# Optimization experiments

Hardware: AMD Instinct MI355X
Metric: run time of the kernel (lower is better)

Reference implementation:

```python
import jax, jax.numpy as jnp
import numpy as np

B, C, N, D, K, M, E, G = 2, 64, 16384, 3, 128, 1, 262144, 3


def setup_inputs() -> dict:
    key = jax.random.key(0)
    ks = jax.random.split(key, 15)
    scale = 1.0 / (C * C)
    return {
        "x": jax.random.normal(ks[0], (B, C, N), jnp.float32),
        "nodes": jax.random.uniform(ks[1], (B, N, D), jnp.float32),
        "node_weights": jax.random.uniform(ks[2], (B, N, M), jnp.float32),
        "geo": jax.random.normal(ks[3], (B, G, N), jnp.float32),
        "directed_edges": jax.random.randint(ks[4], (B, E, 2), 0, N, jnp.int32),
        "edge_gradient_weights": 0.1 * jax.random.normal(ks[5], (B, E, D), jnp.float32),
        "modes": jax.random.normal(ks[6], (K, D, M), jnp.float32),
        "weights_c": scale * jax.random.uniform(ks[7], (C, C, K, M), jnp.float32),
        "weights_s": scale * jax.random.uniform(ks[8], (C, C, K, M), jnp.float32),
        "weights_0": scale * jax.random.uniform(ks[9], (C, C, 1, M), jnp.float32),
        "W": jax.random.normal(ks[10], (C, C), jnp.float32) / np.sqrt(C),
        "gw": jax.random.normal(ks[11], (C, C * D), jnp.float32) / np.sqrt(C * D),
        "geo_wx": jax.random.normal(ks[12], (C, G), jnp.float32) / np.sqrt(G),
        "wx": jax.random.normal(ks[13], (C, C), jnp.float32) / np.sqrt(C),
        "w2": jax.random.normal(ks[14], (C, C), jnp.float32) / np.sqrt(C),
    }


def reference(x, nodes, node_weights, geo, directed_edges, edge_gradient_weights,
              modes, weights_c, weights_s, weights_0, W, gw, geo_wx, wx, w2):
    # ---- Fourier bases: cos(kx), sin(kx), 1 -------------------------------
    temp = jnp.einsum('bxd,kdw->bxkw', nodes, modes)          # [B,N,K,M]
    bases_c, bases_s = jnp.cos(temp), jnp.sin(temp)
    b, n = temp.shape[0], temp.shape[1]
    bases_0 = jnp.ones((b, n, 1, temp.shape[3]), temp.dtype)
    nw = node_weights[:, :, None, :]                          # quadrature weights
    wb_c, wb_s, wb_0 = bases_c * nw, bases_s * nw, bases_0 * nw

    # ---- Spectral convolution (non-uniform Fourier neural layer) ----------
    x_c = jnp.einsum('bix,bxkw->bikw', x, wb_c)
    x_s = -jnp.einsum('bix,bxkw->bikw', x, wb_s)
    x_0 = jnp.einsum('bix,bxkw->bikw', x, wb_0)
    f_c = jnp.einsum('bikw,iokw->bokw', x_c, weights_c) - jnp.einsum('bikw,iokw->bokw', x_s, weights_s)
    f_s = jnp.einsum('bikw,iokw->bokw', x_s, weights_c) + jnp.einsum('bikw,iokw->bokw', x_c, weights_s)
    f_0 = jnp.einsum('bikw,iokw->bokw', x_0, weights_0)
    x1 = (jnp.einsum('bokw,bxkw->box', f_0, bases_0)
          + 2.0 * jnp.einsum('bokw,bxkw->box', f_c, bases_c)
          - 2.0 * jnp.einsum('bokw,bxkw->box', f_s, bases_s))

    # ---- Pointwise linear W ----------------------------------------------
    x2 = jnp.einsum('oi,bix->box', W, x)

    # ---- Least-squares gradient via edge gather + scatter-add -------------
    fT = jnp.transpose(x, (0, 2, 1))                          # [B,N,C]
    tgt, src = directed_edges[..., 0], directed_edges[..., 1]  # [B,E]
    f_src = jnp.take_along_axis(fT, src[:, :, None], axis=1)   # [B,E,C]
    f_tgt = jnp.take_along_axis(fT, tgt[:, :, None], axis=1)
    df = f_src - f_tgt
    # message[b,e,c,d] = w[b,e,d] * df[b,e,c], flattened c-major -> [B,E,C*D]
    msg = (df[..., :, None] * edge_gradient_weights[..., None, :]).reshape(b, tgt.shape[1], -1)
    gradf = jnp.zeros((b, n, msg.shape[-1]), msg.dtype).at[jnp.arange(b)[:, None], tgt].add(msg)
    x3 = jnp.einsum('og,bng->bon', gw, gradf)                  # [B,C,N]

    # ---- Geo embedding: w2 @ (softsign(geo_wx@geo) * (wx@x)) --------------
    h = jax.nn.soft_sign(jnp.einsum('og,bgx->box', geo_wx, geo)) * jnp.einsum('oi,bix->box', wx, x)
    x4 = jnp.einsum('oi,bix->box', w2, h)

    return jax.nn.gelu(x1 + x2 + x3 + x4, approximate=False)
```

## Files before the change

kernel.cpp:

```cpp
#include <hip/hip_runtime.h>
#include <hip/hip_fp16.h>
#include <math.h>

#define BB 2
#define CC 64
#define NN 16384
#define DD 3
#define KK 128
#define EE 262144
#define GG 3
#define PP 128
#define PP2 64
#define LL (NN/PP)
#define KTOT 576

typedef short bf16x8 __attribute__((ext_vector_type(8)));
typedef float f32x4  __attribute__((ext_vector_type(4)));

__device__ __forceinline__ short f2bf(float f) {
    unsigned u = __float_as_uint(f);
    u += 0x7FFF + ((u >> 16) & 1);
    return (short)(u >> 16);
}
__device__ __forceinline__ float bf2f(unsigned short u) {
    return __uint_as_float(((unsigned)u) << 16);
}

constexpr size_t OFF_XB   = 0;
constexpr size_t OFF_PC   = OFF_XB   + (size_t)BB*NN*32;
constexpr size_t OFF_PS   = OFF_PC   + (size_t)BB*PP*CC*KK;
constexpr size_t OFF_BIN4 = OFF_PC;
constexpr size_t OFF_AC   = OFF_PS   + (size_t)BB*PP*CC*KK;
constexpr size_t OFF_AS   = OFF_AC   + (size_t)BB*CC*KK;
constexpr size_t OFF_F0   = OFF_AS   + (size_t)BB*CC*KK;
constexpr size_t OFF_X0   = OFF_F0   + (size_t)BB*CC;
constexpr size_t OFF_CNT  = OFF_X0   + (size_t)BB*CC;
constexpr size_t OFF_OFFS = OFF_CNT  + (size_t)BB*NN;
constexpr size_t OFF_RANK = OFF_OFFS + (size_t)BB*NN;
constexpr size_t OFF_GRB  = OFF_RANK + (size_t)BB*EE;
constexpr size_t OFF_APAN = OFF_GRB  + (size_t)BB*NN*96;
constexpr size_t OFF_GWXT = OFF_APAN + (size_t)BB*KTOT*CC/2;

#define S_B0 (BB*PP2*4)
#define S_B1 (S_B0 + (BB*EE)/256)
#define S_B2 (S_B1 + BB*(NN/64))
#define S_B3 (S_B2 + BB*CC)
#define S_B4 (S_B3 + 48)
__global__ void __launch_bounds__(256) k1(const float* __restrict__ x,
                                          const float* __restrict__ nwt,
                                          const int* __restrict__ edges,
                                          const float* __restrict__ W,
                                          const float* __restrict__ gw,
                                          const float* __restrict__ geo_wx,
                                          const float* __restrict__ w2,
                                          const float* __restrict__ nodes,
                                          const float* __restrict__ modes,
                                          unsigned short* __restrict__ xB,
                                          float* __restrict__ x0,
                                          int* __restrict__ counts,
                                          int* __restrict__ rank,
                                          float* __restrict__ gwxT,
                                          short* __restrict__ ApanB,
                                          float* __restrict__ pc,
                                          float* __restrict__ ps) {
    int blk = blockIdx.x;
    int tid = threadIdx.x;
    __shared__ __align__(16) char smem[36864];
    if (blk < S_B0) {
        short* Axw = (short*)smem;
        short* Bc  = (short*)(smem + 17408);
        short* Bsn = (short*)(smem + 17408 + 8704);
        float* ndl = (float*)(smem + 17408 + 8704 + 8704);
        int bc = blk;
        int b = bc >> 8;
        int rem = bc & 255;
        int chunk2 = rem >> 2;
        int kt = rem & 3;
        int k0 = kt * 32;
        int lane = tid & 63;
        int w = tid >> 6;
        int col = lane & 15;
        int quad = lane >> 4;
        int wk = w & 1;
        int wi = w >> 1;

        f32x4 ac[2], as4[2];
#pragma unroll
        for (int it = 0; it < 2; it++)
#pragma unroll
            for (int r = 0; r < 4; r++) { ac[it][r] = 0.f; as4[it][r] = 0.f; }

        for (int h = 0; h < 2; h++) {
            int nbase = chunk2*256 + h*128;
            if (h) __syncthreads();
            for (int e = tid; e < 128*3; e += 256) ndl[e] = nodes[((size_t)b*NN + nbase)*3 + e];
#pragma unroll
            for (int s = 0; s < 8; s++) {
                int e = tid + s*256;
                int i = e >> 5, seg = e & 31;
                float4 xv = *(const float4*)&x[((size_t)b*CC + i)*NN + nbase + seg*4];
                float4 wv = *(const float4*)&nwt[(size_t)b*NN + nbase + seg*4];
                unsigned lo = (unsigned)(unsigned short)f2bf(xv.x*wv.x)
                            | ((unsigned)(unsigned short)f2bf(xv.y*wv.y) << 16);
                unsigned hi = (unsigned)(unsigned short)f2bf(xv.z*wv.z)
                            | ((unsigned)(unsigned short)f2bf(xv.w*wv.w) << 16);
                *(uint2*)&Axw[i*136 + seg*4] = make_uint2(lo, hi);
            }
            __syncthreads();
#pragma unroll
            for (int s = 0; s < 16; s++) {
                int e = tid + s*256;
                int n = e & 127, kl = e >> 7;
                int k = k0 + kl;
                float t = ndl[n*3+0]*modes[k*3+0] + ndl[n*3+1]*modes[k*3+1]
                        + ndl[n*3+2]*modes[k*3+2];
                Bc [kl*136 + n] = f2bf(__cosf(t));
                Bsn[kl*136 + n] = f2bf(__sinf(t));
            }
            __syncthreads();

            int rowB = (wk*16 + col)*136;
#pragma unroll
            for (int ns = 0; ns < 4; ns++) {
                int koff = ns*32 + quad*8;
                bf16x8 bcf = *(bf16x8*)&Bc [rowB + koff];
                bf16x8 bsf = *(bf16x8*)&Bsn[rowB + koff];
#pragma unroll
                for (int it = 0; it < 2; it++) {
                    int itile = wi*2 + it;
                    bf16x8 af = *(bf16x8*)&Axw[(itile*16 + col)*136 + koff];
                    ac[it]  = __builtin_amdgcn_mfma_f32_16x16x32_bf16(af, bcf, ac[it], 0, 0, 0);
                    as4[it] = __builtin_amdgcn_mfma_f32_16x16x32_bf16(af, bsf, as4[it], 0, 0, 0);
                }
            }
        }
        int base = (b*PP2 + chunk2)*CC;
        int kw = k0 + wk*16 + col;
#pragma unroll
        for (int it = 0; it < 2; it++) {
#pragma unroll
            for (int r = 0; r < 4; r++) {
                int i = (wi*2 + it)*16 + quad*4 + r;
                pc[(size_t)(base + i)*KK + kw] = ac[it][r];
                ps[(size_t)(base + i)*KK + kw] = as4[it][r];
            }
        }
    } else if (blk < S_B1) {
        int idx = (blk - S_B0)*256 + tid;
        int tgt = edges[(size_t)idx*2 + 0];
        int b = idx / EE;
        rank[idx] = atomicAdd(&counts[b*NN + tgt], 1);
    } else if (blk < S_B2) {
        float (*tile)[65] = (float (*)[65])smem;
        int tb = blk - S_B1;
        int b = tb / (NN/64);
        int n0 = (tb % (NN/64)) * 64;
        int c = tid & 63, r4 = tid >> 6;
        for (int rr = 0; rr < 16; rr++) {
            int i = r4*16 + rr;
            tile[i][c] = x[((size_t)b*CC + i)*NN + n0 + c];
        }
        __syncthreads();
        for (int rr = 0; rr < 16; rr++) {
            int nn = r4*16 + rr;
            xB[((size_t)b*NN + n0 + nn)*64 + c] = (unsigned short)f2bf(tile[c][nn]);
        }
    } else if (blk < S_B3) {
        float* red = (float*)smem;
        int bi = blk - S_B2;
        int b = bi >> 6, i = bi & 63;
        const float4* __restrict__ xr = (const float4*)&x[((size_t)b*CC + i)*NN];
        const float4* __restrict__ wr = (const float4*)&nwt[(size_t)b*NN];
        float s = 0.f;
        for (int t = tid; t < NN/4; t += 256) {
            float4 xv = xr[t];
            float4 wv = wr[t];
            s += xv.x*wv.x + xv.y*wv.y + xv.z*wv.z + xv.w*wv.w;
        }
        red[tid] = s;
        __syncthreads();
        for (int off = 128; off > 0; off >>= 1) {
            if (tid < off) red[tid] += red[tid+off];
            __syncthreads();
        }
        if (tid == 0) x0[b*CC + i] = red[0];
    } else {
        int idx = (blk - S_B3)*256 + tid;
        if (idx < CC*CC) {
            int j = idx>>6, o = idx&63;
            short wv  = f2bf(W[o*CC+j]);
            short w2v = f2bf(w2[o*CC+j]);
            ApanB[((size_t)(0*CC+o))*KTOT + 256 + j] = wv;
            ApanB[((size_t)(1*CC+o))*KTOT + 256 + j] = wv;
            ApanB[((size_t)(0*CC+o))*KTOT + 320 + j] = w2v;
            ApanB[((size_t)(1*CC+o))*KTOT + 320 + j] = w2v;
        }
        if (idx < CC*CC*DD) {
            int g = idx>>6, o = idx&63;
            short gv = f2bf(gw[o*(CC*DD)+g]);
            ApanB[((size_t)(0*CC+o))*KTOT + 384 + g] = gv;
            ApanB[((size_t)(1*CC+o))*KTOT + 384 + g] = gv;
        }
        if (idx < GG*CC) { int g = idx>>6, i = idx&63; gwxT[idx] = geo_wx[i*GG+g]; }
    }
}

__global__ void __launch_bounds__(256) k2(const float* __restrict__ pc, const float* __restrict__ ps,
                                          float* __restrict__ Ac, float* __restrict__ As,
                                          const int* __restrict__ counts,
                                          int* __restrict__ offsets) {
    int blk = blockIdx.x;
    int tid = threadIdx.x;
    if (blk < 1024) {
        int idx = blk*16 + (tid >> 4);
        int sub = tid & 15;
        if (idx >= BB*CC*KK) return;
        int b = idx / (CC*KK);
        int r = idx % (CC*KK);
        float sc = 0.f, ss = 0.f;
        for (int ch = sub; ch < PP2; ch += 16) {
            size_t o = ((size_t)(b*PP2 + ch)*CC)*KK + r;
            sc += pc[o]; ss += ps[o];
        }
        sc += __shfl_xor(sc, 1); sc += __shfl_xor(sc, 2);
        sc += __shfl_xor(sc, 4); sc += __shfl_xor(sc, 8);
        ss += __shfl_xor(ss, 1); ss += __shfl_xor(ss, 2);
        ss += __shfl_xor(ss, 4); ss += __shfl_xor(ss, 8);
        if (sub == 0) { Ac[idx] = sc; As[idx] = ss; }
    } else {
        int b = blk - 1024;
        __shared__ int part[256];
        int base = b*NN + tid*64;
        int s = 0;
        for (int j = 0; j < 64; j++) s += counts[base + j];
        part[tid] = s;
        __syncthreads();
        for (int off = 1; off < 256; off <<= 1) {
            int v = (tid >= off) ? part[tid - off] : 0;
            __syncthreads();
            part[tid] += v;
            __syncthreads();
        }
        int excl = part[tid] - s;
        for (int j = 0; j < 64; j++) {
            int c = counts[base + j];
            offsets[base + j] = excl;
            excl += c;
        }
    }
}

__global__ void __launch_bounds__(256) k3(const float* __restrict__ Ac, const float* __restrict__ As_,
                                          const float* __restrict__ wc, const float* __restrict__ wsw,
                                          const float* __restrict__ w0, const float* __restrict__ x0,
                                          const int* __restrict__ edges, const float* __restrict__ egw,
                                          const int* __restrict__ offs, const int* __restrict__ rank,
                                          float4* __restrict__ bin4,
                                          short* __restrict__ ApanB, float* __restrict__ f0) {
    int idx = blockIdx.x;
    int tid = threadIdx.x;
    if (idx >= BB*CC*2) {
        int e = (idx - BB*CC*2)*256 + tid;
        int b = e / EE;
        int tgt = edges[(size_t)e*2+0];
        int src = edges[(size_t)e*2+1];
        const float* __restrict__ ew = &egw[(size_t)e*3];
        float e0 = ew[0], e1 = ew[1], e2 = ew[2];
        int pos = offs[b*NN+tgt] + rank[e];
        bin4[(size_t)b*EE + pos] = make_float4(__int_as_float(src), e0, e1, e2);
        return;
    }
    int b = idx / (CC*2);
    int rem = idx % (CC*2);
    int o = rem >> 1, khalf = rem & 1;
    int kl = tid & 63, ig = tid >> 6;
    int k = khalf*64 + kl;
    float fc = 0.f, fs = 0.f;
    for (int ii = 0; ii < 16; ii++) {
        int i = ig*16 + ii;
        float a_c = Ac[(b*CC+i)*KK + k];
        float a_s = As_[(b*CC+i)*KK + k];
        float wcc = wc[((size_t)(i*CC+o))*KK + k];
        float wss = wsw[((size_t)(i*CC+o))*KK + k];
        fc += a_c*wcc + a_s*wss;
        fs += a_c*wss - a_s*wcc;
    }
    __shared__ float rc[256], rs[256];
    __shared__ float f0s[64];
    rc[tid] = fc; rs[tid] = fs;
    if (khalf == 0 && tid < 64) f0s[tid] = x0[b*CC + tid] * w0[tid*CC + o];
    __syncthreads();
    if (ig == 0) {
        fc = rc[kl] + rc[64+kl] + rc[128+kl] + rc[192+kl];
        fs = rs[kl] + rs[64+kl] + rs[128+kl] + rs[192+kl];
        unsigned pk = (unsigned)(unsigned short)f2bf(2.f*fc)
                    | ((unsigned)(unsigned short)f2bf(-2.f*fs) << 16);
        ((unsigned*)ApanB)[((size_t)(b*CC + o))*(KTOT/2) + k] = pk;
    }
    if (khalf == 0 && tid == 0) {
        float acc = 0.f;
        for (int i = 0; i < 64; i++) acc += f0s[i];
        f0[b*CC+o] = acc;
    }
}

__global__ void __launch_bounds__(512, 8) k_eg(const unsigned short* __restrict__ xB,
                                               const int* __restrict__ offsets,
                                               const float4* __restrict__ bin4,
                                               const float* __restrict__ nodes,
                                               const float* __restrict__ modes,
                                               const float* __restrict__ geo,
                                               const short* __restrict__ ApanB,
                                               const float* __restrict__ f0,
                                               const float* __restrict__ wx,
                                               const float* __restrict__ gwxT,
                                               float* __restrict__ out) {
    int blk = blockIdx.x;
    int b  = blk >> 9;
    int n0 = (blk & 511) * 32;
    int tid = threadIdx.x;
    int lane = tid & 63;
    int w = tid >> 6;
    int wr = w >> 1;
    int wc = w & 1;
    int col  = lane & 15;
    int quad = lane >> 4;
    int quad8 = quad * 8;
    int quad4 = quad * 4;

    __shared__ __align__(16) char smem[37776];
    short* As = (short*)smem;
    short* Bs = (short*)(smem + 9216);
    short* Ws = (short*)(smem + 13824);
    unsigned short* gradfL = (unsigned short*)(smem + 23040);
    float* ndl  = (float*)(smem + 36864);
    float* geo3 = (float*)(smem + 37248);
    int* soff   = (int*)(smem + 37632);

    if (tid < 96) ndl[tid]  = nodes[((size_t)b*NN + n0)*3 + tid];
    if (tid < 96) geo3[tid] = geo[((size_t)b*GG + (tid >> 5))*NN + n0 + (tid & 31)];
    if (tid >= 128 && tid < 161) {
        int idx = n0 + tid - 128;
        soff[tid - 128] = (idx < NN) ? offsets[b*NN + idx] : EE;
    }
    for (int e = tid; e < 4096; e += 512) {
        int i = e >> 6, j = e & 63;
        Ws[i*72 + j] = f2bf(wx[i*64 + j]);
    }
    f32x4 acc, xwa;
#pragma unroll
    for (int r = 0; r < 4; r++) { acc[r] = f0[b*CC + wr*16 + quad4 + r]; xwa[r] = 0.f; }
    __syncthreads();

    const unsigned short* __restrict__ xBb = xB + (size_t)b*NN*64 + lane;
    const float4* __restrict__ binb = bin4 + (size_t)b*EE;
    for (int q = 0; q < 4; q++) {
        int nl = w*4 + q;
        int js = soff[nl], je = soff[nl+1];
        float a0 = 0.f, a1 = 0.f, a2 = 0.f, s0 = 0.f, s1 = 0.f, s2 = 0.f;
#pragma unroll 4
        for (int j = js; j < je; j++) {
            float4 e = binb[j];
            int src = __float_as_int(e.x);
            float xs = bf2f(xBb[(size_t)src*64]);
            a0 = fmaf(xs, e.y, a0);
            a1 = fmaf(xs, e.z, a1);
            a2 = fmaf(xs, e.w, a2);
            s0 += e.y; s1 += e.z; s2 += e.w;
        }
        float xtgt = bf2f(xBb[(size_t)(n0 + nl)*64]);
        float fv0 = a0 - xtgt*s0;
        float fv1 = a1 - xtgt*s1;
        float fv2 = a2 - xtgt*s2;
        int g0 = lane*3;
        gradfL[(g0>>6)*2304 + nl*72 + (g0&63)] = (unsigned short)f2bf(fv0);
        int g1 = g0 + 1;
        gradfL[(g1>>6)*2304 + nl*72 + (g1&63)] = (unsigned short)f2bf(fv1);
        int g2 = g0 + 2;
        gradfL[(g2>>6)*2304 + nl*72 + (g2&63)] = (unsigned short)f2bf(fv2);
    }

    const short* __restrict__ Ab = ApanB + ((size_t)b*CC)*KTOT;

    for (int c = 0; c < 9; c++) {
        __syncthreads();
        {
            int o = tid >> 3, seg = tid & 7;
            *(uint4*)&As[o*72 + seg*8] =
                *(const uint4*)&Ab[(size_t)o*KTOT + c*64 + seg*8];
        }
        if (c < 4) {
#pragma unroll
            for (int s = 0; s < 2; s++) {
                int e = tid + s*512;
                int n = e >> 5, kpl = e & 31;
                int kp = c*32 + kpl;
                float t = ndl[n*3+0]*modes[kp*3+0] + ndl[n*3+1]*modes[kp*3+1]
                        + ndl[n*3+2]*modes[kp*3+2];
                unsigned pk = (unsigned)(unsigned short)f2bf(__cosf(t))
                            | ((unsigned)(unsigned short)f2bf(__sinf(t)) << 16);
                ((unsigned*)Bs)[n*36 + kpl] = pk;
            }
        } else if (c == 4) {
            if (tid < 256) {
                int n = tid >> 3, seg = tid & 7;
                *(uint4*)&Bs[n*72 + seg*8] =
                    *(const uint4*)&xB[((size_t)(b*NN + n0 + n))*64 + seg*8];
            }
        } else if (c == 5) {
            int n = wc*16 + col;
            float gv0 = geo3[n], gv1 = geo3[32+n], gv2 = geo3[64+n];
#pragma unroll
            for (int r = 0; r < 4; r++) {
                int i = wr*16 + quad4 + r;
                float t = gwxT[i]*gv0 + gwxT[64+i]*gv1 + gwxT[128+i]*gv2;
                float ssv = t / (1.f + fabsf(t));
                Bs[n*72 + i] = f2bf(ssv * xwa[r]);
            }
        }
        __syncthreads();
        const short* Bbase = (c >= 6) ? (const short*)&gradfL[(size_t)(c-6)*2304] : Bs;
        int rowA = (wr*16 + col) * 72;
        int rowB = (wc*16 + col) * 72;
#pragma unroll
        for (int ko = 0; ko < 2; ko++) {
            int koff = ko*32 + quad8;
            bf16x8 af = *(bf16x8*)&As[rowA + koff];
            bf16x8 bfv = *(bf16x8*)&Bbase[rowB + koff];
            acc = __builtin_amdgcn_mfma_f32_16x16x32_bf16(af, bfv, acc, 0, 0, 0);
            if (c == 4) {
                bf16x8 wf = *(bf16x8*)&Ws[rowA + koff];
                xwa = __builtin_amdgcn_mfma_f32_16x16x32_bf16(wf, bfv, xwa, 0, 0, 0);
            }
        }
    }
#pragma unroll
    for (int r = 0; r < 4; r++) {
        int o = wr*16 + quad4 + r;
        float v = acc[r];
        float g = 0.5f * v * (1.f + erff(v * 0.70710678118654752f));
        out[((size_t)b*CC + o)*NN + n0 + wc*16 + col] = g;
    }
}

extern "C" void kernel_launch(void* const* d_in, const int* in_sizes, int n_in,
                              void* d_out, int out_size, void* d_ws, size_t ws_size,
                              hipStream_t stream) {
    const float* x      = (const float*)d_in[0];
    const float* nodes  = (const float*)d_in[1];
    const float* nwt    = (const float*)d_in[2];
    const float* geo    = (const float*)d_in[3];
    const int*   edges  = (const int*)d_in[4];
    const float* egw    = (const float*)d_in[5];
    const float* modes  = (const float*)d_in[6];
    const float* wc     = (const float*)d_in[7];
    const float* wsw    = (const float*)d_in[8];
    const float* w0     = (const float*)d_in[9];
    const float* W      = (const float*)d_in[10];
    const float* gw     = (const float*)d_in[11];
    const float* geo_wx = (const float*)d_in[12];
    const float* wx     = (const float*)d_in[13];
    const float* w2     = (const float*)d_in[14];

    float* ws   = (float*)d_ws;
    unsigned short* xB  = (unsigned short*)(ws + OFF_XB);
    float* pc   = ws + OFF_PC;
    float* ps   = ws + OFF_PS;
    float* Ac   = ws + OFF_AC;
    float* As_  = ws + OFF_AS;
    float* f0   = ws + OFF_F0;
    float* x0   = ws + OFF_X0;
    int*  counts = (int*)(ws + OFF_CNT);
    int*  offs   = (int*)(ws + OFF_OFFS);
    int*  rank   = (int*)(ws + OFF_RANK);
    float4* bin4 = (float4*)(ws + OFF_BIN4);
    short* ApanB  = (short*)(ws + OFF_APAN);
    float* gwxT   = ws + OFF_GWXT;
    float* out  = (float*)d_out;

    hipMemsetAsync(counts, 0, (size_t)(BB*NN)*sizeof(int), stream);

    k1 <<<S_B4, 256, 0, stream>>>(x, nwt, edges, W, gw, geo_wx, w2, nodes, modes,
                                  xB, x0, counts, rank, gwxT, ApanB, pc, ps);
    k2 <<<1024 + BB, 256, 0, stream>>>(pc, ps, Ac, As_, counts, offs);
    k3 <<<BB*CC*2 + (BB*EE)/256, 256, 0, stream>>>(Ac, As_, wc, wsw, w0, x0,
                                                   edges, egw, offs, rank, bin4, ApanB, f0);
    k_eg <<<BB*(NN/32), 512, 0, stream>>>(xB, offs, bin4, nodes, modes, geo,
                                          ApanB, f0, wx, gwxT, out);
}
```

Baseline: 181.7 us.

## Merge four kernel launches into one cooperative persistent kernel with grid syncs

```diff
diff --git a/kernel.cpp b/kernel.cpp
--- a/kernel.cpp
+++ b/kernel.cpp
@@ -1,6 +1,9 @@
 #include <hip/hip_runtime.h>
+#include <hip/hip_cooperative_groups.h>
 #include <hip/hip_fp16.h>
 #include <math.h>
+
+namespace cg = cooperative_groups;
 
 #define BB 2
 #define CC 64
@@ -9,9 +12,7 @@
 #define KK 128
 #define EE 262144
 #define GG 3
-#define PP 128
 #define PP2 64
-#define LL (NN/PP)
 #define KTOT 576
 
 typedef short bf16x8 __attribute__((ext_vector_type(8)));
@@ -28,9 +29,9 @@
 
 constexpr size_t OFF_XB   = 0;
 constexpr size_t OFF_PC   = OFF_XB   + (size_t)BB*NN*32;
-constexpr size_t OFF_PS   = OFF_PC   + (size_t)BB*PP*CC*KK;
+constexpr size_t OFF_PS   = OFF_PC   + (size_t)BB*128*CC*KK;
 constexpr size_t OFF_BIN4 = OFF_PC;
-constexpr size_t OFF_AC   = OFF_PS   + (size_t)BB*PP*CC*KK;
+constexpr size_t OFF_AC   = OFF_PS   + (size_t)BB*128*CC*KK;
 constexpr size_t OFF_AS   = OFF_AC   + (size_t)BB*CC*KK;
 constexpr size_t OFF_F0   = OFF_AS   + (size_t)BB*CC*KK;
 constexpr size_t OFF_X0   = OFF_F0   + (size_t)BB*CC;
@@ -41,405 +42,379 @@
 constexpr size_t OFF_APAN = OFF_GRB  + (size_t)BB*NN*96;
 constexpr size_t OFF_GWXT = OFF_APAN + (size_t)BB*KTOT*CC/2;
 
-#define S_B0 (BB*PP2*4)
-#define S_B1 (S_B0 + (BB*EE)/256)
-#define S_B2 (S_B1 + BB*(NN/64))
-#define S_B3 (S_B2 + BB*CC)
-#define S_B4 (S_B3 + 48)
-__global__ void __launch_bounds__(256) k1(const float* __restrict__ x,
-                                          const float* __restrict__ nwt,
-                                          const int* __restrict__ edges,
-                                          const float* __restrict__ W,
-                                          const float* __restrict__ gw,
-                                          const float* __restrict__ geo_wx,
-                                          const float* __restrict__ w2,
-                                          const float* __restrict__ nodes,
-                                          const float* __restrict__ modes,
-                                          unsigned short* __restrict__ xB,
-                                          float* __restrict__ x0,
-                                          int* __restrict__ counts,
-                                          int* __restrict__ rank,
-                                          float* __restrict__ gwxT,
-                                          short* __restrict__ ApanB,
-                                          float* __restrict__ pc,
-                                          float* __restrict__ ps) {
-    int blk = blockIdx.x;
-    int tid = threadIdx.x;
-    __shared__ __align__(16) char smem[36864];
-    if (blk < S_B0) {
-        short* Axw = (short*)smem;
-        short* Bc  = (short*)(smem + 17408);
-        short* Bsn = (short*)(smem + 17408 + 8704);
-        float* ndl = (float*)(smem + 17408 + 8704 + 8704);
-        int bc = blk;
-        int b = bc >> 8;
-        int rem = bc & 255;
-        int chunk2 = rem >> 2;
-        int kt = rem & 3;
-        int k0 = kt * 32;
-        int lane = tid & 63;
-        int w = tid >> 6;
-        int col = lane & 15;
-        int quad = lane >> 4;
-        int wk = w & 1;
-        int wi = w >> 1;
-
-        f32x4 ac[2], as4[2];
-#pragma unroll
-        for (int it = 0; it < 2; it++)
-#pragma unroll
-            for (int r = 0; r < 4; r++) { ac[it][r] = 0.f; as4[it][r] = 0.f; }
-
-        for (int h = 0; h < 2; h++) {
-            int nbase = chunk2*256 + h*128;
-            if (h) __syncthreads();
-            for (int e = tid; e < 128*3; e += 256) ndl[e] = nodes[((size_t)b*NN + nbase)*3 + e];
-#pragma unroll
-            for (int s = 0; s < 8; s++) {
-                int e = tid + s*256;
-                int i = e >> 5, seg = e & 31;
-                float4 xv = *(const float4*)&x[((size_t)b*CC + i)*NN + nbase + seg*4];
-                float4 wv = *(const float4*)&nwt[(size_t)b*NN + nbase + seg*4];
-                unsigned lo = (unsigned)(unsigned short)f2bf(xv.x*wv.x)
-                            | ((unsigned)(unsigned short)f2bf(xv.y*wv.y) << 16);
-                unsigned hi = (unsigned)(unsigned short)f2bf(xv.z*wv.z)
-                            | ((unsigned)(unsigned short)f2bf(xv.w*wv.w) << 16);
-                *(uint2*)&Axw[i*136 + seg*4] = make_uint2(lo, hi);
-            }
-            __syncthreads();
-#pragma unroll
-            for (int s = 0; s < 16; s++) {
-                int e = tid + s*256;
-                int n = e & 127, kl = e >> 7;
-                int k = k0 + kl;
-                float t = ndl[n*3+0]*modes[k*3+0] + ndl[n*3+1]*modes[k*3+1]
-                        + ndl[n*3+2]*modes[k*3+2];
-                Bc [kl*136 + n] = f2bf(__cosf(t));
-                Bsn[kl*136 + n] = f2bf(__sinf(t));
-            }
-            __syncthreads();
-
-            int rowB = (wk*16 + col)*136;
-#pragma unroll
-            for (int ns = 0; ns < 4; ns++) {
-                int koff = ns*32 + quad*8;
-                bf16x8 bcf = *(bf16x8*)&Bc [rowB + koff];
-                bf16x8 bsf = *(bf16x8*)&Bsn[rowB + koff];
-#pragma unroll
-                for (int it = 0; it < 2; it++) {
-                    int itile = wi*2 + it;
-                    bf16x8 af = *(bf16x8*)&Axw[(itile*16 + col)*136 + koff];
-                    ac[it]  = __builtin_amdgcn_mfma_f32_16x16x32_bf16(af, bcf, ac[it], 0, 0, 0);
-                    as4[it] = __builtin_amdgcn_mfma_f32_16x16x32_bf16(af, bsf, as4[it], 0, 0, 0);
-                }
-            }
-        }
-        int base = (b*PP2 + chunk2)*CC;
-        int kw = k0 + wk*16 + col;
-#pragma unroll
-        for (int it = 0; it < 2; it++) {
-#pragma unroll
-            for (int r = 0; r < 4; r++) {
-                int i = (wi*2 + it)*16 + quad*4 + r;
-                pc[(size_t)(base + i)*KK + kw] = ac[it][r];
-                ps[(size_t)(base + i)*KK + kw] = as4[it][r];
-            }
-        }
-    } else if (blk < S_B1) {
-        int idx = (blk - S_B0)*256 + tid;
-        int tgt = edges[(size_t)idx*2 + 0];
-        int b = idx / EE;
-        rank[idx] = atomicAdd(&counts[b*NN + tgt], 1);
-    } else if (blk < S_B2) {
-        float (*tile)[65] = (float (*)[65])smem;
-        int tb = blk - S_B1;
-        int b = tb / (NN/64);
-        int n0 = (tb % (NN/64)) * 64;
-        int c = tid & 63, r4 = tid >> 6;
-        for (int rr = 0; rr < 16; rr++) {
-            int i = r4*16 + rr;
-            tile[i][c] = x[((size_t)b*CC + i)*NN + n0 + c];
-        }
-        __syncthreads();
-        for (int rr = 0; rr < 16; rr++) {
-            int nn = r4*16 + rr;
-            xB[((size_t)b*NN + n0 + nn)*64 + c] = (unsigned short)f2bf(tile[c][nn]);
-        }
-    } else if (blk < S_B3) {
-        float* red = (float*)smem;
-        int bi = blk - S_B2;
-        int b = bi >> 6, i = bi & 63;
-        const float4* __restrict__ xr = (const float4*)&x[((size_t)b*CC + i)*NN];
-        const float4* __restrict__ wr = (const float4*)&nwt[(size_t)b*NN];
-        float s = 0.f;
-        for (int t = tid; t < NN/4; t += 256) {
-            float4 xv = xr[t];
-            float4 wv = wr[t];
-            s += xv.x*wv.x + xv.y*wv.y + xv.z*wv.z + xv.w*wv.w;
-        }
-        red[tid] = s;
-        __syncthreads();
-        for (int off = 128; off > 0; off >>= 1) {
-            if (tid < off) red[tid] += red[tid+off];
-            __syncthreads();
-        }
-        if (tid == 0) x0[b*CC + i] = red[0];
-    } else {
-        int idx = (blk - S_B3)*256 + tid;
-        if (idx < CC*CC) {
-            int j = idx>>6, o = idx&63;
-            short wv  = f2bf(W[o*CC+j]);
-            short w2v = f2bf(w2[o*CC+j]);
-            ApanB[((size_t)(0*CC+o))*KTOT + 256 + j] = wv;
-            ApanB[((size_t)(1*CC+o))*KTOT + 256 + j] = wv;
-            ApanB[((size_t)(0*CC+o))*KTOT + 320 + j] = w2v;
-            ApanB[((size_t)(1*CC+o))*KTOT + 320 + j] = w2v;
-        }
-        if (idx < CC*CC*DD) {
-            int g = idx>>6, o = idx&63;
-            short gv = f2bf(gw[o*(CC*DD)+g]);
-            ApanB[((size_t)(0*CC+o))*KTOT + 384 + g] = gv;
-            ApanB[((size_t)(1*CC+o))*KTOT + 384 + g] = gv;
-        }
-        if (idx < GG*CC) { int g = idx>>6, i = idx&63; gwxT[idx] = geo_wx[i*GG+g]; }
-    }
-}
-
-__global__ void __launch_bounds__(256) k2(const float* __restrict__ pc, const float* __restrict__ ps,
-                                          float* __restrict__ Ac, float* __restrict__ As,
-                                          const int* __restrict__ counts,
-                                          int* __restrict__ offsets) {
-    int blk = blockIdx.x;
-    int tid = threadIdx.x;
-    if (blk < 1024) {
-        int idx = blk*16 + (tid >> 4);
-        int sub = tid & 15;
-        if (idx >= BB*CC*KK) return;
-        int b = idx / (CC*KK);
-        int r = idx % (CC*KK);
-        float sc = 0.f, ss = 0.f;
-        for (int ch = sub; ch < PP2; ch += 16) {
-            size_t o = ((size_t)(b*PP2 + ch)*CC)*KK + r;
-            sc += pc[o]; ss += ps[o];
-        }
-        sc += __shfl_xor(sc, 1); sc += __shfl_xor(sc, 2);
-        sc += __shfl_xor(sc, 4); sc += __shfl_xor(sc, 8);
-        ss += __shfl_xor(ss, 1); ss += __shfl_xor(ss, 2);
-        ss += __shfl_xor(ss, 4); ss += __shfl_xor(ss, 8);
-        if (sub == 0) { Ac[idx] = sc; As[idx] = ss; }
-    } else {
-        int b = blk - 1024;
-        __shared__ int part[256];
-        int base = b*NN + tid*64;
-        int s = 0;
-        for (int j = 0; j < 64; j++) s += counts[base + j];
-        part[tid] = s;
-        __syncthreads();
-        for (int off = 1; off < 256; off <<= 1) {
-            int v = (tid >= off) ? part[tid - off] : 0;
-            __syncthreads();
-            part[tid] += v;
-            __syncthreads();
-        }
-        int excl = part[tid] - s;
-        for (int j = 0; j < 64; j++) {
-            int c = counts[base + j];
-            offsets[base + j] = excl;
-            excl += c;
-        }
-    }
-}
-
-__global__ void __launch_bounds__(256) k3(const float* __restrict__ Ac, const float* __restrict__ As_,
-                                          const float* __restrict__ wc, const float* __restrict__ wsw,
-                                          const float* __restrict__ w0, const float* __restrict__ x0,
-                                          const int* __restrict__ edges, const float* __restrict__ egw,
-                                          const int* __restrict__ offs, const int* __restrict__ rank,
-                                          float4* __restrict__ bin4,
-                                          short* __restrict__ ApanB, float* __restrict__ f0) {
-    int idx = blockIdx.x;
-    int tid = threadIdx.x;
-    if (idx >= BB*CC*2) {
-        int e = (idx - BB*CC*2)*256 + tid;
-        int b = e / EE;
-        int tgt = edges[(size_t)e*2+0];
-        int src = edges[(size_t)e*2+1];
-        const float* __restrict__ ew = &egw[(size_t)e*3];
-        float e0 = ew[0], e1 = ew[1], e2 = ew[2];
-        int pos = offs[b*NN+tgt] + rank[e];
-        bin4[(size_t)b*EE + pos] = make_float4(__int_as_float(src), e0, e1, e2);
-        return;
-    }
-    int b = idx / (CC*2);
-    int rem = idx % (CC*2);
-    int o = rem >> 1, khalf = rem & 1;
-    int kl = tid & 63, ig = tid >> 6;
-    int k = khalf*64 + kl;
-    float fc = 0.f, fs = 0.f;
-    for (int ii = 0; ii < 16; ii++) {
-        int i = ig*16 + ii;
-        float a_c = Ac[(b*CC+i)*KK + k];
-        float a_s = As_[(b*CC+i)*KK + k];
-        float wcc = wc[((size_t)(i*CC+o))*KK + k];
-        float wss = wsw[((size_t)(i*CC+o))*KK + k];
-        fc += a_c*wcc + a_s*wss;
-        fs += a_c*wss - a_s*wcc;
-    }
-    __shared__ float rc[256], rs[256];
-    __shared__ float f0s[64];
-    rc[tid] = fc; rs[tid] = fs;
-    if (khalf == 0 && tid < 64) f0s[tid] = x0[b*CC + tid] * w0[tid*CC + o];
-    __syncthreads();
-    if (ig == 0) {
-        fc = rc[kl] + rc[64+kl] + rc[128+kl] + rc[192+kl];
-        fs = rs[kl] + rs[64+kl] + rs[128+kl] + rs[192+kl];
-        unsigned pk = (unsigned)(unsigned short)f2bf(2.f*fc)
-                    | ((unsigned)(unsigned short)f2bf(-2.f*fs) << 16);
-        ((unsigned*)ApanB)[((size_t)(b*CC + o))*(KTOT/2) + k] = pk;
-    }
-    if (khalf == 0 && tid == 0) {
-        float acc = 0.f;
-        for (int i = 0; i < 64; i++) acc += f0s[i];
-        f0[b*CC+o] = acc;
-    }
-}
-
-__global__ void __launch_bounds__(512, 8) k_eg(const unsigned short* __restrict__ xB,
-                                               const int* __restrict__ offsets,
-                                               const float4* __restrict__ bin4,
-                                               const float* __restrict__ nodes,
-                                               const float* __restrict__ modes,
-                                               const float* __restrict__ geo,
-                                               const short* __restrict__ ApanB,
-                                               const float* __restrict__ f0,
-                                               const float* __restrict__ wx,
-                                               const float* __restrict__ gwxT,
-                                               float* __restrict__ out) {
-    int blk = blockIdx.x;
-    int b  = blk >> 9;
-    int n0 = (blk & 511) * 32;
+#define U_KA  (BB*PP2*4)
+#define U_ED  ((BB*EE)/512)
+#define U_TR  (BB*(NN/64))
+#define U_X0  (BB*CC)
+#define U_WT  24
+#define U1 (U_KA + U_ED + U_TR + U_X0 + U_WT)
+#define U2 (512 + BB)
+#define U3 (BB*CC + (BB*EE)/512)
+#define U4 (BB*(NN/32))
+
+__global__ void __launch_bounds__(512, 8)
+mega(const float* __restrict__ x, const float* __restrict__ nwt,
+     const int* __restrict__ edges, const float* __restrict__ egw,
+     const float* __restrict__ W, const float* __restrict__ gw,
+     const float* __restrict__ geo_wx, const float* __restrict__ w2,
+     const float* __restrict__ nodes, const float* __restrict__ modes,
+     const float* __restrict__ geo, const float* __restrict__ wcw,
+     const float* __restrict__ wsw, const float* __restrict__ w0,
+     const float* __restrict__ wx,
+     unsigned short* __restrict__ xB, float* __restrict__ x0v,
+     int* __restrict__ counts, int* __restrict__ rank,
+     float* __restrict__ gwxT, short* __restrict__ ApanB,
+     float* __restrict__ pc, float* __restrict__ ps,
+     float* __restrict__ Ac, float* __restrict__ As_,
+     float* __restrict__ f0, int* __restrict__ offsets,
+     float4* __restrict__ bin4, float* __restrict__ out) {
+    cg::grid_group gridg = cg::this_grid();
+    int NB = gridDim.x;
     int tid = threadIdx.x;
     int lane = tid & 63;
     int w = tid >> 6;
-    int wr = w >> 1;
-    int wc = w & 1;
-    int col  = lane & 15;
-    int quad = lane >> 4;
-    int quad8 = quad * 8;
-    int quad4 = quad * 4;
-
     __shared__ __align__(16) char smem[37776];
-    short* As = (short*)smem;
-    short* Bs = (short*)(smem + 9216);
-    short* Ws = (short*)(smem + 13824);
-    unsigned short* gradfL = (unsigned short*)(smem + 23040);
-    float* ndl  = (float*)(smem + 36864);
-    float* geo3 = (float*)(smem + 37248);
-    int* soff   = (int*)(smem + 37632);
-
-    if (tid < 96) ndl[tid]  = nodes[((size_t)b*NN + n0)*3 + tid];
-    if (tid < 96) geo3[tid] = geo[((size_t)b*GG + (tid >> 5))*NN + n0 + (tid & 31)];
-    if (tid >= 128 && tid < 161) {
-        int idx = n0 + tid - 128;
-        soff[tid - 128] = (idx < NN) ? offsets[b*NN + idx] : EE;
-    }
-    for (int e = tid; e < 4096; e += 512) {
-        int i = e >> 6, j = e & 63;
-        Ws[i*72 + j] = f2bf(wx[i*64 + j]);
-    }
-    f32x4 acc, xwa;
-#pragma unroll
-    for (int r = 0; r < 4; r++) { acc[r] = f0[b*CC + wr*16 + quad4 + r]; xwa[r] = 0.f; }
-    __syncthreads();
-
-    const unsigned short* __restrict__ xBb = xB + (size_t)b*NN*64 + lane;
-    const float4* __restrict__ binb = bin4 + (size_t)b*EE;
-    for (int q = 0; q < 4; q++) {
-        int nl = w*4 + q;
-        int js = soff[nl], je = soff[nl+1];
-        float a0 = 0.f, a1 = 0.f, a2 = 0.f, s0 = 0.f, s1 = 0.f, s2 = 0.f;
-#pragma unroll 4
-        for (int j = js; j < je; j++) {
-            float4 e = binb[j];
-            int src = __float_as_int(e.x);
-            float xs = bf2f(xBb[(size_t)src*64]);
-            a0 = fmaf(xs, e.y, a0);
-            a1 = fmaf(xs, e.z, a1);
-            a2 = fmaf(xs, e.w, a2);
-            s0 += e.y; s1 += e.z; s2 += e.w;
-        }
-        float xtgt = bf2f(xBb[(size_t)(n0 + nl)*64]);
-        float fv0 = a0 - xtgt*s0;
-        float fv1 = a1 - xtgt*s1;
-        float fv2 = a2 - xtgt*s2;
-        int g0 = lane*3;
-        gradfL[(g0>>6)*2304 + nl*72 + (g0&63)] = (unsigned short)f2bf(fv0);
-        int g1 = g0 + 1;
-        gradfL[(g1>>6)*2304 + nl*72 + (g1&63)] = (unsigned short)f2bf(fv1);
-        int g2 = g0 + 2;
-        gradfL[(g2>>6)*2304 + nl*72 + (g2&63)] = (unsigned short)f2bf(fv2);
-    }
-
-    const short* __restrict__ Ab = ApanB + ((size_t)b*CC)*KTOT;
-
-    for (int c = 0; c < 9; c++) {
+
+    for (int u = blockIdx.x; u < U1; u += NB) {
         __syncthreads();
-        {
-            int o = tid >> 3, seg = tid & 7;
-            *(uint4*)&As[o*72 + seg*8] =
-                *(const uint4*)&Ab[(size_t)o*KTOT + c*64 + seg*8];
-        }
-        if (c < 4) {
-#pragma unroll
-            for (int s = 0; s < 2; s++) {
-                int e = tid + s*512;
-                int n = e >> 5, kpl = e & 31;
-                int kp = c*32 + kpl;
-                float t = ndl[n*3+0]*modes[kp*3+0] + ndl[n*3+1]*modes[kp*3+1]
-                        + ndl[n*3+2]*modes[kp*3+2];
-                unsigned pk = (unsigned)(unsigned short)f2bf(__cosf(t))
-                            | ((unsigned)(unsigned short)f2bf(__sinf(t)) << 16);
-                ((unsigned*)Bs)[n*36 + kpl] = pk;
-            }
-        } else if (c == 4) {
-            if (tid < 256) {
-                int n = tid >> 3, seg = tid & 7;
-                *(uint4*)&Bs[n*72 + seg*8] =
-                    *(const uint4*)&xB[((size_t)(b*NN + n0 + n))*64 + seg*8];
-            }
-        } else if (c == 5) {
-            int n = wc*16 + col;
-            float gv0 = geo3[n], gv1 = geo3[32+n], gv2 = geo3[64+n];
+        if (u < U_KA) {
+            short* Axw = (short*)smem;
+            short* Bc  = (short*)(smem + 17408);
+            short* Bsn = (short*)(smem + 17408 + 8704);
+            float* ndl = (float*)(smem + 17408 + 8704 + 8704);
+            int b = u >> 8;
+            int rem = u & 255;
+            int chunk2 = rem >> 2;
+            int kt = rem & 3;
+            int k0 = kt * 32;
+            int col = lane & 15;
+            int quad = lane >> 4;
+            int wk = w & 1;
+            int wi = w >> 1;
+            f32x4 ac, as4;
+#pragma unroll
+            for (int r = 0; r < 4; r++) { ac[r] = 0.f; as4[r] = 0.f; }
+            for (int h = 0; h < 2; h++) {
+                int nbase = chunk2*256 + h*128;
+                if (h) __syncthreads();
+                for (int e = tid; e < 384; e += 512) ndl[e] = nodes[((size_t)b*NN + nbase)*3 + e];
+#pragma unroll
+                for (int s = 0; s < 4; s++) {
+                    int e = tid + s*512;
+                    int i = e >> 5, seg = e & 31;
+                    float4 xv = *(const float4*)&x[((size_t)b*CC + i)*NN + nbase + seg*4];
+                    float4 wv = *(const float4*)&nwt[(size_t)b*NN + nbase + seg*4];
+                    unsigned lo = (unsigned)(unsigned short)f2bf(xv.x*wv.x)
+                                | ((unsigned)(unsigned short)f2bf(xv.y*wv.y) << 16);
+                    unsigned hi = (unsigned)(unsigned short)f2bf(xv.z*wv.z)
+                                | ((unsigned)(unsigned short)f2bf(xv.w*wv.w) << 16);
+                    *(uint2*)&Axw[i*136 + seg*4] = make_uint2(lo, hi);
+                }
+                __syncthreads();
+#pragma unroll
+                for (int s = 0; s < 8; s++) {
+                    int e = tid + s*512;
+                    int n = e & 127, kl = e >> 7;
+                    int k = k0 + kl;
+                    float t = ndl[n*3+0]*modes[k*3+0] + ndl[n*3+1]*modes[k*3+1]
+                            + ndl[n*3+2]*modes[k*3+2];
+                    Bc [kl*136 + n] = f2bf(__cosf(t));
+                    Bsn[kl*136 + n] = f2bf(__sinf(t));
+                }
+                __syncthreads();
+                int rowB = (wk*16 + col)*136;
+#pragma unroll
+                for (int ns = 0; ns < 4; ns++) {
+                    int koff = ns*32 + quad*8;
+                    bf16x8 bcf = *(bf16x8*)&Bc [rowB + koff];
+                    bf16x8 bsf = *(bf16x8*)&Bsn[rowB + koff];
+                    bf16x8 af = *(bf16x8*)&Axw[(wi*16 + col)*136 + koff];
+                    ac  = __builtin_amdgcn_mfma_f32_16x16x32_bf16(af, bcf, ac, 0, 0, 0);
+                    as4 = __builtin_amdgcn_mfma_f32_16x16x32_bf16(af, bsf, as4, 0, 0, 0);
+                }
+            }
+            int base = (b*PP2 + chunk2)*CC;
+            int kw = k0 + wk*16 + col;
 #pragma unroll
             for (int r = 0; r < 4; r++) {
-                int i = wr*16 + quad4 + r;
-                float t = gwxT[i]*gv0 + gwxT[64+i]*gv1 + gwxT[128+i]*gv2;
-                float ssv = t / (1.f + fabsf(t));
-                Bs[n*72 + i] = f2bf(ssv * xwa[r]);
-            }
-        }
-        __syncthreads();
-        const short* Bbase = (c >= 6) ? (const short*)&gradfL[(size_t)(c-6)*2304] : Bs;
-        int rowA = (wr*16 + col) * 72;
-        int rowB = (wc*16 + col) * 72;
-#pragma unroll
-        for (int ko = 0; ko < 2; ko++) {
-            int koff = ko*32 + quad8;
-            bf16x8 af = *(bf16x8*)&As[rowA + koff];
-            bf16x8 bfv = *(bf16x8*)&Bbase[rowB + koff];
-            acc = __builtin_amdgcn_mfma_f32_16x16x32_bf16(af, bfv, acc, 0, 0, 0);
-            if (c == 4) {
-                bf16x8 wf = *(bf16x8*)&Ws[rowA + koff];
-                xwa = __builtin_amdgcn_mfma_f32_16x16x32_bf16(wf, bfv, xwa, 0, 0, 0);
-            }
+                int i = wi*16 + quad*4 + r;
+                pc[(size_t)(base + i)*KK + kw] = ac[r];
+                ps[(size_t)(base + i)*KK + kw] = as4[r];
+            }
+        } else if (u < U_KA + U_ED) {
+            int idx = (u - U_KA)*512 + tid;
+            int tgt = edges[(size_t)idx*2 + 0];
+            int b = idx / EE;
+            rank[idx] = atomicAdd(&counts[b*NN + tgt], 1);
+        } else if (u < U_KA + U_ED + U_TR) {
+            float (*tile)[65] = (float (*)[65])smem;
+            int tb = u - (U_KA + U_ED);
+            int b = tb / (NN/64);
+            int n0 = (tb % (NN/64)) * 64;
+            int c = tid & 63, r8 = tid >> 6;
+            for (int rr = 0; rr < 8; rr++) {
+                int i = r8*8 + rr;
+                tile[i][c] = x[((size_t)b*CC + i)*NN + n0 + c];
+            }
+            __syncthreads();
+            for (int rr = 0; rr < 8; rr++) {
+                int nn = r8*8 + rr;
+                xB[((size_t)b*NN + n0 + nn)*64 + c] = (unsigned short)f2bf(tile[c][nn]);
+            }
+        } else if (u < U_KA + U_ED + U_TR + U_X0) {
+            float* red = (float*)smem;
+            int bi = u - (U_KA + U_ED + U_TR);
+            int b = bi >> 6, i = bi & 63;
+            const float4* __restrict__ xr = (const float4*)&x[((size_t)b*CC + i)*NN];
+            const float4* __restrict__ wr = (const float4*)&nwt[(size_t)b*NN];
+            float s = 0.f;
+            for (int t = tid; t < NN/4; t += 512) {
+                float4 xv = xr[t];
+                float4 wv = wr[t];
+                s += xv.x*wv.x + xv.y*wv.y + xv.z*wv.z + xv.w*wv.w;
+            }
+            red[tid] = s;
+            __syncthreads();
+            for (int off = 256; off > 0; off >>= 1) {
+                if (tid < off) red[tid] += red[tid+off];
+                __syncthreads();
+            }
+            if (tid == 0) x0v[b*CC + i] = red[0];
+        } else {
+            int idx = (u - (U_KA + U_ED + U_TR + U_X0))*512 + tid;
+            if (idx < CC*CC) {
+                int j = idx>>6, o = idx&63;
+                short wv  = f2bf(W[o*CC+j]);
+                short w2v = f2bf(w2[o*CC+j]);
+                ApanB[((size_t)(0*CC+o))*KTOT + 256 + j] = wv;
+                ApanB[((size_t)(1*CC+o))*KTOT + 256 + j] = wv;
+                ApanB[((size_t)(0*CC+o))*KTOT + 320 + j] = w2v;
+                ApanB[((size_t)(1*CC+o))*KTOT + 320 + j] = w2v;
+            }
+            if (idx < CC*CC*DD) {
+                int g = idx>>6, o = idx&63;
+                short gv = f2bf(gw[o*(CC*DD)+g]);
+                ApanB[((size_t)(0*CC+o))*KTOT + 384 + g] = gv;
+                ApanB[((size_t)(1*CC+o))*KTOT + 384 + g] = gv;
+            }
+            if (idx < GG*CC) { int g = idx>>6, i = idx&63; gwxT[idx] = geo_wx[i*GG+g]; }
         }
     }
-#pragma unroll
-    for (int r = 0; r < 4; r++) {
-        int o = wr*16 + quad4 + r;
-        float v = acc[r];
-        float g = 0.5f * v * (1.f + erff(v * 0.70710678118654752f));
-        out[((size_t)b*CC + o)*NN + n0 + wc*16 + col] = g;
+    gridg.sync();
+
+    for (int u = blockIdx.x; u < U2; u += NB) {
+        __syncthreads();
+        if (u < 512) {
+            int idx = u*32 + (tid >> 4);
+            int sub = tid & 15;
+            int b = idx / (CC*KK);
+            int r = idx % (CC*KK);
+            float sc = 0.f, ss = 0.f;
+            for (int ch = sub; ch < PP2; ch += 16) {
+                size_t o = ((size_t)(b*PP2 + ch)*CC)*KK + r;
+                sc += pc[o]; ss += ps[o];
+            }
+            sc += __shfl_xor(sc, 1); sc += __shfl_xor(sc, 2);
+            sc += __shfl_xor(sc, 4); sc += __shfl_xor(sc, 8);
+            ss += __shfl_xor(ss, 1); ss += __shfl_xor(ss, 2);
+            ss += __shfl_xor(ss, 4); ss += __shfl_xor(ss, 8);
+            if (sub == 0) { Ac[idx] = sc; As_[idx] = ss; }
+        } else {
+            int b = u - 512;
+            int* part = (int*)smem;
+            int base = b*NN + tid*32;
+            int s = 0;
+            for (int j = 0; j < 32; j++) s += counts[base + j];
+            part[tid] = s;
+            __syncthreads();
+            for (int off = 1; off < 512; off <<= 1) {
+                int v = (tid >= off) ? part[tid - off] : 0;
+                __syncthreads();
+                part[tid] += v;
+                __syncthreads();
+            }
+            int excl = part[tid] - s;
+            for (int j = 0; j < 32; j++) {
+                int c = counts[base + j];
+                offsets[base + j] = excl;
+                excl += c;
+            }
+        }
+    }
+    gridg.sync();
+
+    for (int u = blockIdx.x; u < U3; u += NB) {
+        __syncthreads();
+        if (u < BB*CC) {
+            float* rc  = (float*)smem;
+            float* rs  = (float*)(smem + 2048);
+            float* f0s = (float*)(smem + 4096);
+            int b = u >> 6, o = u & 63;
+            int khalf = tid >> 8;
+            int t2 = tid & 255;
+            int kl = t2 & 63, ig = t2 >> 6;
+            int k = khalf*64 + kl;
+            float fc = 0.f, fs = 0.f;
+            for (int ii = 0; ii < 16; ii++) {
+                int i = ig*16 + ii;
+                float a_c = Ac[(b*CC+i)*KK + k];
+                float a_s = As_[(b*CC+i)*KK + k];
+                float wcc = wcw[((size_t)(i*CC+o))*KK + k];
+                float wss = wsw[((size_t)(i*CC+o))*KK + k];
+                fc += a_c*wcc + a_s*wss;
+                fs += a_c*wss - a_s*wcc;
+            }
+            rc[tid] = fc; rs[tid] = fs;
+            if (tid < 64) f0s[tid] = x0v[b*CC + tid] * w0[tid*CC + o];
+            __syncthreads();
+            if (ig == 0) {
+                int tb = khalf*256;
+                fc = rc[tb+kl] + rc[tb+64+kl] + rc[tb+128+kl] + rc[tb+192+kl];
+                fs = rs[tb+kl] + rs[tb+64+kl] + rs[tb+128+kl] + rs[tb+192+kl];
+                unsigned pk = (unsigned)(unsigned short)f2bf(2.f*fc)
+                            | ((unsigned)(unsigned short)f2bf(-2.f*fs) << 16);
+                ((unsigned*)ApanB)[((size_t)(b*CC + o))*(KTOT/2) + k] = pk;
+            }
+            if (tid == 0) {
+                float acc2 = 0.f;
+                for (int i = 0; i < 64; i++) acc2 += f0s[i];
+                f0[b*CC+o] = acc2;
+            }
+        } else {
+            int e = (u - BB*CC)*512 + tid;
+            int b = e / EE;
+            int tgt = edges[(size_t)e*2+0];
+            int src = edges[(size_t)e*2+1];
+            const float* __restrict__ ew = &egw[(size_t)e*3];
+            float e0 = ew[0], e1 = ew[1], e2 = ew[2];
+            int pos = offsets[b*NN+tgt] + rank[e];
+            bin4[(size_t)b*EE + pos] = make_float4(__int_as_float(src), e0, e1, e2);
+        }
+    }
+    gridg.sync();
+
+    {
+        short* As = (short*)smem;
+        short* Bs = (short*)(smem + 9216);
+        short* Ws = (short*)(smem + 13824);
+        unsigned short* gradfL = (unsigned short*)(smem + 23040);
+        float* ndl  = (float*)(smem + 36864);
+        float* geo3 = (float*)(smem + 37248);
+        int* soff   = (int*)(smem + 37632);
+        int wr = w >> 1;
+        int wc = w & 1;
+        int col  = lane & 15;
+        int quad = lane >> 4;
+        int quad8 = quad * 8;
+        int quad4 = quad * 4;
+        for (int u = blockIdx.x; u < U4; u += NB) {
+            __syncthreads();
+            int b  = u >> 9;
+            int n0 = (u & 511) * 32;
+            if (tid < 96) ndl[tid]  = nodes[((size_t)b*NN + n0)*3 + tid];
+            if (tid < 96) geo3[tid] = geo[((size_t)b*GG + (tid >> 5))*NN + n0 + (tid & 31)];
+            if (tid >= 128 && tid < 161) {
+                int idx = n0 + tid - 128;
+                soff[tid - 128] = (idx < NN) ? offsets[b*NN + idx] : EE;
+            }
+            for (int e = tid; e < 4096; e += 512) {
+                int i = e >> 6, j = e & 63;
+                Ws[i*72 + j] = f2bf(wx[i*64 + j]);
+            }
+            f32x4 acc, xwa;
+#pragma unroll
+            for (int r = 0; r < 4; r++) { acc[r] = f0[b*CC + wr*16 + quad4 + r]; xwa[r] = 0.f; }
+            __syncthreads();
+
+            const unsigned short* __restrict__ xBb = xB + (size_t)b*NN*64 + lane;
+            const float4* __restrict__ binb = bin4 + (size_t)b*EE;
+            for (int q = 0; q < 4; q++) {
+                int nl = w*4 + q;
+                int js = soff[nl], je = soff[nl+1];
+                float a0 = 0.f, a1 = 0.f, a2 = 0.f, s0 = 0.f, s1 = 0.f, s2 = 0.f;
+#pragma unroll 4
+                for (int j = js; j < je; j++) {
+                    float4 e = binb[j];
+                    int src = __float_as_int(e.x);
+                    float xs = bf2f(xBb[(size_t)src*64]);
+                    a0 = fmaf(xs, e.y, a0);
+                    a1 = fmaf(xs, e.z, a1);
+                    a2 = fmaf(xs, e.w, a2);
+                    s0 += e.y; s1 += e.z; s2 += e.w;
+                }
+                float xtgt = bf2f(xBb[(size_t)(n0 + nl)*64]);
+                float fv0 = a0 - xtgt*s0;
+                float fv1 = a1 - xtgt*s1;
+                float fv2 = a2 - xtgt*s2;
+                int g0 = lane*3;
+                gradfL[(g0>>6)*2304 + nl*72 + (g0&63)] = (unsigned short)f2bf(fv0);
+                int g1 = g0 + 1;
+                gradfL[(g1>>6)*2304 + nl*72 + (g1&63)] = (unsigned short)f2bf(fv1);
+                int g2 = g0 + 2;
+                gradfL[(g2>>6)*2304 + nl*72 + (g2&63)] = (unsigned short)f2bf(fv2);
+            }
+
+            const short* __restrict__ Ab = ApanB + ((size_t)b*CC)*KTOT;
+            for (int c = 0; c < 9; c++) {
+                __syncthreads();
+                {
+                    int o = tid >> 3, seg = tid & 7;
+                    *(uint4*)&As[o*72 + seg*8] =
+                        *(const uint4*)&Ab[(size_t)o*KTOT + c*64 + seg*8];
+                }
+                if (c < 4) {
+#pragma unroll
+                    for (int s = 0; s < 2; s++) {
+                        int e = tid + s*512;
+                        int n = e >> 5, kpl = e & 31;
+                        int kp = c*32 + kpl;
+                        float t = ndl[n*3+0]*modes[kp*3+0] + ndl[n*3+1]*modes[kp*3+1]
+                                + ndl[n*3+2]*modes[kp*3+2];
+                        unsigned pk = (unsigned)(unsigned short)f2bf(__cosf(t))
+                                    | ((unsigned)(unsigned short)f2bf(__sinf(t)) << 16);
+                        ((unsigned*)Bs)[n*36 + kpl] = pk;
+                    }
+                } else if (c == 4) {
+                    if (tid < 256) {
+                        int n = tid >> 3, seg = tid & 7;
+                        *(uint4*)&Bs[n*72 + seg*8] =
+                            *(const uint4*)&xB[((size_t)(b*NN + n0 + n))*64 + seg*8];
+                    }
+                } else if (c == 5) {
+                    int n = wc*16 + col;
+                    float gv0 = geo3[n], gv1 = geo3[32+n], gv2 = geo3[64+n];
+#pragma unroll
+                    for (int r = 0; r < 4; r++) {
+                        int i = wr*16 + quad4 + r;
+                        float t = gwxT[i]*gv0 + gwxT[64+i]*gv1 + gwxT[128+i]*gv2;
+                        float ssv = t / (1.f + fabsf(t));
+                        Bs[n*72 + i] = f2bf(ssv * xwa[r]);
+                    }
+                }
+                __syncthreads();
+                const short* Bbase = (c >= 6) ? (const short*)&gradfL[(size_t)(c-6)*2304] : Bs;
+                int rowA = (wr*16 + col) * 72;
+                int rowB = (wc*16 + col) * 72;
+#pragma unroll
+                for (int ko = 0; ko < 2; ko++) {
+                    int koff = ko*32 + quad8;
+                    bf16x8 af = *(bf16x8*)&As[rowA + koff];
+                    bf16x8 bfv = *(bf16x8*)&Bbase[rowB + koff];
+                    acc = __builtin_amdgcn_mfma_f32_16x16x32_bf16(af, bfv, acc, 0, 0, 0);
+                    if (c == 4) {
+                        bf16x8 wf = *(bf16x8*)&Ws[rowA + koff];
+                        xwa = __builtin_amdgcn_mfma_f32_16x16x32_bf16(wf, bfv, xwa, 0, 0, 0);
+                    }
+                }
+            }
+#pragma unroll
+            for (int r = 0; r < 4; r++) {
+                int o = wr*16 + quad4 + r;
+                float v = acc[r];
+                float g = 0.5f * v * (1.f + erff(v * 0.70710678118654752f));
+                out[((size_t)b*CC + o)*NN + n0 + wc*16 + col] = g;
+            }
+        }
     }
 }
 
@@ -453,7 +428,7 @@
     const int*   edges  = (const int*)d_in[4];
     const float* egw    = (const float*)d_in[5];
     const float* modes  = (const float*)d_in[6];
-    const float* wc     = (const float*)d_in[7];
+    const float* wcw    = (const float*)d_in[7];
     const float* wsw    = (const float*)d_in[8];
     const float* w0     = (const float*)d_in[9];
     const float* W      = (const float*)d_in[10];
@@ -469,7 +444,7 @@
     float* Ac   = ws + OFF_AC;
     float* As_  = ws + OFF_AS;
     float* f0   = ws + OFF_F0;
-    float* x0   = ws + OFF_X0;
+    float* x0v  = ws + OFF_X0;
     int*  counts = (int*)(ws + OFF_CNT);
     int*  offs   = (int*)(ws + OFF_OFFS);
     int*  rank   = (int*)(ws + OFF_RANK);
@@ -480,11 +455,27 @@
 
     hipMemsetAsync(counts, 0, (size_t)(BB*NN)*sizeof(int), stream);
 
-    k1 <<<S_B4, 256, 0, stream>>>(x, nwt, edges, W, gw, geo_wx, w2, nodes, modes,
-                                  xB, x0, counts, rank, gwxT, ApanB, pc, ps);
-    k2 <<<1024 + BB, 256, 0, stream>>>(pc, ps, Ac, As_, counts, offs);
-    k3 <<<BB*CC*2 + (BB*EE)/256, 256, 0, stream>>>(Ac, As_, wc, wsw, w0, x0,
-                                                   edges, egw, offs, rank, bin4, ApanB, f0);
-    k_eg <<<BB*(NN/32), 512, 0, stream>>>(xB, offs, bin4, nodes, modes, geo,
-                                          ApanB, f0, wx, gwxT, out);
+    static int s_nb = 0;
+    if (s_nb == 0) {
+        int bpc = 0;
+        hipError_t err = hipOccupancyMaxActiveBlocksPerMultiprocessor(
+            &bpc, (const void*)mega, 512, 0);
+        if (err != hipSuccess || bpc < 1) bpc = 1;
+        s_nb = bpc * 256;
+        if (s_nb > 1024) s_nb = 1024;
+        if (s_nb < 1) s_nb = 1;
+    }
+
+    void* args[] = {
+        (void*)&x, (void*)&nwt, (void*)&edges, (void*)&egw,
+        (void*)&W, (void*)&gw, (void*)&geo_wx, (void*)&w2,
+        (void*)&nodes, (void*)&modes, (void*)&geo, (void*)&wcw,
+        (void*)&wsw, (void*)&w0, (void*)&wx,
+        (void*)&xB, (void*)&x0v, (void*)&counts, (void*)&rank,
+        (void*)&gwxT, (void*)&ApanB, (void*)&pc, (void*)&ps,
+        (void*)&Ac, (void*)&As_, (void*)&f0, (void*)&offs,
+        (void*)&bin4, (void*)&out
+    };
+    hipLaunchCooperativeKernel((const void*)mega, dim3(s_nb), dim3(512),
+                               args, 0, stream);
 }
```

Result: slower. 485.7 us (+167.4%).
